# Kernel optimization log

Measured on AMD Instinct MI355X. Metric: run time of the kernel, lower is better.

Reference implementation:

```python
import jax, jax.numpy as jnp
import numpy as np

D_MODEL = 1024
NUM_HEADS = 16
D_HEAD = D_MODEL // NUM_HEADS
THETA = 10000.0
B, S = 2, 2048


def setup_inputs() -> dict:
    key = jax.random.key(0)
    ks = jax.random.split(key, 5)
    std = np.sqrt(2.0 / (D_MODEL + D_MODEL))
    x = jax.random.normal(ks[0], (B, S, D_MODEL), dtype=jnp.float32)
    Wq = jax.random.normal(ks[1], (D_MODEL, D_MODEL), dtype=jnp.float32) * std
    Wk = jax.random.normal(ks[2], (D_MODEL, D_MODEL), dtype=jnp.float32) * std
    Wv = jax.random.normal(ks[3], (D_MODEL, D_MODEL), dtype=jnp.float32) * std
    Wo = jax.random.normal(ks[4], (D_MODEL, D_MODEL), dtype=jnp.float32) * std
    token_positions = jnp.arange(S, dtype=jnp.int32)
    return {"x": x, "Wq": Wq, "Wk": Wk, "Wv": Wv, "Wo": Wo,
            "token_positions": token_positions}


def _apply_rope(t, token_positions):
    # t: [B, H, S, d_head]; interleaved (even/odd) RoPE
    dh = t.shape[-1]
    inv_freq = 1.0 / (THETA ** (jnp.arange(0, dh, 2, dtype=jnp.float32) / dh))
    freqs = token_positions.astype(jnp.float32)[:, None] * inv_freq  # [S, dh/2]
    cos = jnp.cos(freqs)  # broadcasts over B, H
    sin = jnp.sin(freqs)
    x1 = t[..., 0::2]
    x2 = t[..., 1::2]
    r1 = x1 * cos - x2 * sin
    r2 = x1 * sin + x2 * cos
    return jnp.stack([r1, r2], axis=-1).reshape(t.shape)


def reference(x, Wq, Wk, Wv, Wo, token_positions):
    b, s, d = x.shape
    h, dh = NUM_HEADS, D_HEAD

    def proj(W):
        y = x @ W.T  # [B, S, D]
        return y.reshape(b, s, h, dh).transpose(0, 2, 1, 3)  # [B, H, S, dh]

    q = _apply_rope(proj(Wq), token_positions)
    k = _apply_rope(proj(Wk), token_positions)
    v = proj(Wv)

    scores = jnp.einsum('bhqd,bhkd->bhqk', q, k) / jnp.sqrt(jnp.float32(dh))
    causal = jnp.tril(jnp.ones((s, s), dtype=bool))
    scores = jnp.where(causal, scores, jnp.float32(-jnp.inf))
    attn = jax.nn.softmax(scores, axis=-1)
    out = jnp.einsum('bhqk,bhkd->bhqd', attn, v)  # [B, H, S, dh]
    out = out.transpose(0, 2, 1, 3).reshape(b, s, d)
    return out @ Wo.T
```

## Files before the change

### kernel.cpp

```cpp
#include <hip/hip_runtime.h>
#include <hip/hip_bf16.h>
#include <math.h>

#define DMODEL 1024
#define NHEAD  16
#define DHEAD  64
#define BATCH  2
#define SEQ    2048
#define MROWS  (BATCH * SEQ)

typedef __attribute__((ext_vector_type(8))) __bf16 bf16x8;
typedef __attribute__((ext_vector_type(4))) float  f32x4;

__device__ __forceinline__ void load16_lds(const ushort* g, ushort* l) {
    __builtin_amdgcn_global_load_lds(
        (const __attribute__((address_space(1))) unsigned int*)g,
        (__attribute__((address_space(3))) unsigned int*)l, 16, 0, 0);
}

__device__ __forceinline__ ushort bf16u(float v) {
    __hip_bfloat16 h = __float2bfloat16(v);
    return *reinterpret_cast<ushort*>(&h);
}

__global__ __launch_bounds__(256)
void cast_f32_bf16(const float* __restrict__ s, ushort* __restrict__ d, int n) {
    const int i = (blockIdx.x * 256 + threadIdx.x) * 8;
    if (i >= n) return;
    const f32x4 a = *reinterpret_cast<const f32x4*>(s + i);
    const f32x4 b = *reinterpret_cast<const f32x4*>(s + i + 4);
    bf16x8 o;
    #pragma unroll
    for (int j = 0; j < 4; j++) { o[j] = (__bf16)a[j]; o[4 + j] = (__bf16)b[j]; }
    *reinterpret_cast<bf16x8*>(d + i) = o;
}

__global__ __launch_bounds__(256)
void cast_w4(const float* __restrict__ w0, const float* __restrict__ w1,
             const float* __restrict__ w2, const float* __restrict__ w3,
             ushort* __restrict__ dst) {
    const float* src = (blockIdx.y == 0) ? w0 : (blockIdx.y == 1) ? w1
                     : (blockIdx.y == 2) ? w2 : w3;
    const int i = (blockIdx.x * 256 + threadIdx.x) * 8;
    const f32x4 a = *reinterpret_cast<const f32x4*>(src + i);
    const f32x4 b = *reinterpret_cast<const f32x4*>(src + i + 4);
    bf16x8 o;
    #pragma unroll
    for (int j = 0; j < 4; j++) { o[j] = (__bf16)a[j]; o[4 + j] = (__bf16)b[j]; }
    *reinterpret_cast<bf16x8*>(dst + (size_t)blockIdx.y * DMODEL * DMODEL + i) = o;
}

__global__ __launch_bounds__(256)
void rope_tab(const int* __restrict__ pos, float2* __restrict__ tab) {
    const int idx = blockIdx.x * 256 + threadIdx.x;
    const int s = idx >> 5;
    const int i = idx & 31;
    const float p = (float)pos[s];
    const float inv = exp2f(-(float)i * 0.41524101186092f);
    float sn, cs;
    sincosf(p * inv, &sn, &cs);
    tab[idx] = make_float2(cs, sn);
}

#define QKV_BARRIER() do { asm volatile("" ::: "memory"); \
                           __builtin_amdgcn_s_barrier(); } while (0)

#define RD4(dst, p_)                                                          \
    _Pragma("unroll")                                                         \
    for (int rr_ = 0; rr_ < 4; rr_++)                                         \
        dst[rr_] = *reinterpret_cast<const bf16x8*>((p_) + rr_ * 512);

#define MFMA_G(AFR, BFR, IOFF)                                                \
    __builtin_amdgcn_s_setprio(1);                                            \
    _Pragma("unroll")                                                         \
    for (int im_ = 0; im_ < 4; im_++)                                         \
        _Pragma("unroll")                                                     \
        for (int jn_ = 0; jn_ < 4; jn_++)                                     \
            acc[(IOFF) + im_][jn_] = __builtin_amdgcn_mfma_f32_16x16x32_bf16( \
                AFR[im_], BFR[jn_], acc[(IOFF) + im_][jn_], 0, 0, 0);         \
    __builtin_amdgcn_s_setprio(0);

__global__ __launch_bounds__(512, 2)
void gemm_qkv(const ushort* __restrict__ A, const ushort* __restrict__ B,
              ushort* __restrict__ C, const float2* __restrict__ tab) {
    __shared__ __align__(16) ushort pool[65536];

    const int orig = blockIdx.y * gridDim.x + blockIdx.x;
    const int xcd  = orig & 7;
    const int ixd  = orig >> 3;
    const int by   = xcd * 2 + (ixd / 12);
    const int bx   = ixd % 12;
    const int m0   = by * 256;
    const int n0   = bx * 256;

    const int tid  = threadIdx.x;
    const int lane = tid & 63;
    const int w    = tid >> 6;
    const int l16  = lane & 15;
    const int quad = lane >> 4;
    const int wm   = (w >> 2) * 128;
    const int wn   = (w & 3) * 64;
    const int chq  = (quad ^ ((l16 & 3) ^ ((l16 & 4) >> 1))) << 3;
    const int srow = tid >> 2;
    const int ssc  = (tid & 3) ^ ((srow & 3) ^ ((srow & 4) >> 1));

    const ushort* gA = A + (size_t)(m0 + srow) * DMODEL + ssc * 8;
    const ushort* gB = B + (size_t)(n0 + srow) * DMODEL + ssc * 8;

    auto stageA = [&](int tt, int ks) {
        const int off = tt * 64 + ks * 32;
        const int lb  = ((tt & 1) << 15) + (ks << 13);
        load16_lds(gA + off,                &pool[lb + tid * 8]);
        load16_lds(gA + 128 * DMODEL + off, &pool[lb + 4096 + tid * 8]);
    };
    auto stageB = [&](int tt, int ks) {
        const int off = tt * 64 + ks * 32;
        const int lb  = ((tt & 1) << 15) + 16384 + (ks << 13);
        load16_lds(gB + off,                &pool[lb + tid * 8]);
        load16_lds(gB + 128 * DMODEL + off, &pool[lb + 4096 + tid * 8]);
    };

    stageA(0, 0); stageB(0, 0);
    stageA(0, 1); stageB(0, 1);
    stageA(1, 0); stageB(1, 0);

    f32x4 acc[8][4];
    #pragma unroll
    for (int i = 0; i < 8; i++)
        #pragma unroll
        for (int j = 0; j < 4; j++) acc[i][j] = (f32x4){0.f, 0.f, 0.f, 0.f};

    asm volatile("s_waitcnt vmcnt(4)" ::: "memory");
    __builtin_amdgcn_s_barrier();

    bf16x8 al[4], ah[4], bc[4], bn[4];

    { const ushort* p = pool + (wm + l16) * 32 + chq;           RD4(al, p); }
    { const ushort* q = pool + 16384 + (wn + l16) * 32 + chq;   RD4(bc, q); }

    #pragma unroll 1
    for (int t = 0; t < 16; t++) {
        const int buf  = (t & 1) << 15;
        const int bufn = buf ^ 32768;
        if (t <= 14) { stageA(t + 1, 1); stageB(t + 1, 1); }
        { const ushort* p = pool + buf + (wm + 64 + l16) * 32 + chq;
          RD4(ah, p); }
        MFMA_G(al, bc, 0);
        { const ushort* p = pool + buf + 8192 + (wm + l16) * 32 + chq;
          RD4(al, p);
          const ushort* q = pool + buf + 16384 + 8192 + (wn + l16) * 32 + chq;
          RD4(bn, q); }
        MFMA_G(ah, bc, 4);
        if (t <= 14) { asm volatile("s_waitcnt vmcnt(4)" ::: "memory"); }
        QKV_BARRIER();
        if (t <= 13) { stageA(t + 2, 0); stageB(t + 2, 0); }
        { const ushort* p = pool + buf + 8192 + (wm + 64 + l16) * 32 + chq;
          RD4(ah, p); }
        MFMA_G(al, bn, 0);
        if (t <= 14) {
            const ushort* p = pool + bufn + (wm + l16) * 32 + chq;
            RD4(al, p);
            const ushort* q = pool + bufn + 16384 + (wn + l16) * 32 + chq;
            RD4(bc, q);
        }
        MFMA_G(ah, bn, 4);
        if (t <= 13)      { asm volatile("s_waitcnt vmcnt(4)" ::: "memory"); }
        else if (t == 14) { asm volatile("s_waitcnt vmcnt(0)" ::: "memory"); }
        QKV_BARRIER();
    }

    const int nbase  = n0 + wn;
    const int tensor = nbase >> 10;
    const int hh     = (nbase & 1023) >> 6;
    if (tensor < 2) {
        ushort* Dt = C + (size_t)tensor * ((size_t)MROWS * DMODEL);
        #pragma unroll
        for (int i = 0; i < 8; i++)
            #pragma unroll
            for (int r = 0; r < 4; r++) {
                const int m  = m0 + wm + i * 16 + quad * 4 + r;
                const int bb = m >> 11;
                const int ss = m & (SEQ - 1);
                const float2* trow = tab + ss * 32;
                #pragma unroll
                for (int j = 0; j < 4; j++) {
                    const int f = j * 16 + l16;
                    const float2 cs = trow[f >> 1];
                    const float val = acc[i][j][r];
                    const float prt = __shfl_xor(val, 1, 64);
                    const float out = (f & 1) ? (prt * cs.y + val * cs.x)
                                              : (val * cs.x - prt * cs.y);
                    Dt[(((size_t)(bb * NHEAD + hh)) * SEQ + ss) * DHEAD + f] =
                        bf16u(out);
                }
            }
    } else {
        ushort* Tw = pool + w * 8192;
        #pragma unroll
        for (int i = 0; i < 8; i++)
            #pragma unroll
            for (int j = 0; j < 4; j++) {
                const int f  = j * 16 + l16;
                const int sx = (f & 7) << 3;
                #pragma unroll
                for (int r = 0; r < 4; r += 2) {
                    const int ml = i * 16 + quad * 4 + r;
                    ushort2 pk;
                    pk.x = bf16u(acc[i][j][r]);
                    pk.y = bf16u(acc[i][j][r + 1]);
                    *reinterpret_cast<ushort2*>(&Tw[f * 128 + (ml ^ sx)]) = pk;
                }
            }
        asm volatile("s_waitcnt lgkmcnt(0)" ::: "memory");
        ushort* Dv = C + 2 * ((size_t)MROWS * DMODEL);
        const int c  = lane & 15;
        const int fb = lane >> 4;
        #pragma unroll
        for (int rr = 0; rr < 16; rr++) {
            const int fl = rr * 4 + fb;
            const uint4 v = *reinterpret_cast<const uint4*>(
                &Tw[fl * 128 + ((c << 3) ^ ((fl & 7) << 3))]);
            *reinterpret_cast<uint4*>(
                &Dv[(size_t)(hh * 64 + fl) * MROWS + m0 + wm + (c << 3)]) = v;
        }
    }
}

__global__ __launch_bounds__(256)
void gemm_out64(const ushort* __restrict__ A, const ushort* __restrict__ B,
                float* __restrict__ C) {
    __shared__ __align__(16) ushort pool[12288];
    ushort* As = pool;
    ushort* Bs = pool + 4096;
    const int tid  = threadIdx.x;
    const int m0   = blockIdx.y * 64;
    const int n0   = blockIdx.x * 128;
    const int lane = tid & 63;
    const int w    = tid >> 6;
    const int l16  = lane & 15;
    const int quad = lane >> 4;
    const int wm   = (w >> 1) * 32;
    const int wn   = (w & 1) * 64;
    const int srow = tid >> 2;
    const int scol = (tid & 3) * 8;

    const int am  = m0 + srow;
    const int abb = am >> 11;
    const int ass = am & (SEQ - 1);
    const size_t abase = ((size_t)(abb * NHEAD)) * SEQ * DHEAD + (size_t)ass * DHEAD;

    f32x4 acc[2][4];
    #pragma unroll
    for (int i = 0; i < 2; i++)
        #pragma unroll
        for (int j = 0; j < 4; j++) acc[i][j] = (f32x4){0.f, 0.f, 0.f, 0.f};

    {
        const int h = scol >> 6, dh = scol & 63;
        load16_lds(A + abase + (size_t)h * SEQ * DHEAD + dh, &As[srow * 32 + scol]);
        #pragma unroll
        for (int half = 0; half < 2; half++) {
            const int row = srow + half * 64;
            load16_lds(B + (size_t)(n0 + row) * DMODEL + scol, &Bs[row * 32 + scol]);
        }
    }

    for (int t = 0; t < 32; t++) {
        const int bf = t & 1;
        __syncthreads();
        if (t + 1 < 32) {
            const int k0 = (t + 1) * 32;
            const int kk = k0 + scol;
            const int h = kk >> 6, dh = kk & 63;
            load16_lds(A + abase + (size_t)h * SEQ * DHEAD + dh,
                       &As[(bf ^ 1) * 2048 + srow * 32 + scol]);
            #pragma unroll
            for (int half = 0; half < 2; half++) {
                const int row = srow + half * 64;
                load16_lds(B + (size_t)(n0 + row) * DMODEL + k0 + scol,
                           &Bs[(bf ^ 1) * 4096 + row * 32 + scol]);
            }
        }
        const int oa = bf * 2048, ob_ = bf * 4096;
        bf16x8 af[2], bfr[4];
        #pragma unroll
        for (int s = 0; s < 2; s++)
            af[s] = *reinterpret_cast<const bf16x8*>(
                &As[oa + (wm + s * 16 + l16) * 32 + quad * 8]);
        #pragma unroll
        for (int s = 0; s < 4; s++)
            bfr[s] = *reinterpret_cast<const bf16x8*>(
                &Bs[ob_ + (wn + s * 16 + l16) * 32 + quad * 8]);
        #pragma unroll
        for (int i = 0; i < 2; i++)
            #pragma unroll
            for (int j = 0; j < 4; j++)
                acc[i][j] = __builtin_amdgcn_mfma_f32_16x16x32_bf16(
                    af[i], bfr[j], acc[i][j], 0, 0, 0);
    }
    #pragma unroll
    for (int i = 0; i < 2; i++)
        #pragma unroll
        for (int r = 0; r < 4; r++) {
            const int m = m0 + wm + i * 16 + quad * 4 + r;
            #pragma unroll
            for (int j = 0; j < 4; j++)
                C[(size_t)m * DMODEL + n0 + wn + j * 16 + l16] = acc[i][j][r];
        }
}

__global__ __launch_bounds__(256)
void attn_mfma6(const ushort* __restrict__ qb, const ushort* __restrict__ kb,
                const ushort* __restrict__ vtg, ushort* __restrict__ ob) {
    __shared__ __align__(16) ushort Ks[2][4096];
    __shared__ __align__(16) ushort Vs[2][4096];
    __shared__ ushort Pb[4][16][72];

    const int bh   = blockIdx.x;
    const int b    = bh >> 4;
    const int h    = bh & 15;
    const int qt   = (gridDim.y - 1) - blockIdx.y;
    const int tid  = threadIdx.x;
    const int w    = tid >> 6;
    const int lane = tid & 63;
    const int l16  = lane & 15;
    const int quad = lane >> 4;
    const size_t base = (size_t)bh * SEQ * DHEAD;

    const int qlo = qt * 64 + w * 16;

    const float SC = 0.125f * 1.44269504088896f;
    bf16x8 qa[2];
    {
        const size_t qo = base + (size_t)(qlo + l16) * DHEAD + quad * 8;
        qa[0] = *reinterpret_cast<const bf16x8*>(qb + qo);
        qa[1] = *reinterpret_cast<const bf16x8*>(qb + qo + 32);
        #pragma unroll
        for (int j = 0; j < 8; j++) {
            qa[0][j] = (__bf16)(SC * (float)qa[0][j]);
            qa[1][j] = (__bf16)(SC * (float)qa[1][j]);
        }
    }

    f32x4 oacc[4];
    #pragma unroll
    for (int s = 0; s < 4; s++) oacc[s] = (f32x4){0.f, 0.f, 0.f, 0.f};
    float l_ = 0.f;

    const int c0 = tid,        r0 = c0 >> 3, g0 = (c0 & 7) ^ (r0 & 7);
    const int c1 = 256 + tid,  r1 = c1 >> 3, g1 = (c1 & 7) ^ (r1 & 7);
    const ushort* kg0 = kb + base + (size_t)r0 * DHEAD + g0 * 8;
    const ushort* kg1 = kb + base + (size_t)r1 * DHEAD + g1 * 8;
    const ushort* vg0 = vtg + (size_t)(h * DHEAD + r0) * MROWS + b * SEQ + g0 * 8;
    const ushort* vg1 = vtg + (size_t)(h * DHEAD + r1) * MROWS + b * SEQ + g1 * 8;

    int koff[2][4];
    #pragma unroll
    for (int half = 0; half < 2; half++)
        #pragma unroll
        for (int sub = 0; sub < 4; sub++)
            koff[half][sub] = (sub * 16 + l16) * 64 +
                              (((half * 4 + quad) ^ (l16 & 7)) * 8);

    load16_lds(kg0, &Ks[0][c0 * 8]);
    load16_lds(kg1, &Ks[0][c1 * 8]);
    load16_lds(vg0, &Vs[0][c0 * 8]);
    load16_lds(vg1, &Vs[0][c1 * 8]);

    const int T = qt + 1;
    for (int t = 0; t < T; t++) {
        const int bf = t & 1;
        __syncthreads();
        if (t + 1 < T) {
            const size_t ko = (size_t)(t + 1) * 64 * DHEAD;
            const int    vo = (t + 1) * 64;
            load16_lds(kg0 + ko, &Ks[bf ^ 1][c0 * 8]);
            load16_lds(kg1 + ko, &Ks[bf ^ 1][c1 * 8]);
            load16_lds(vg0 + vo, &Vs[bf ^ 1][c0 * 8]);
            load16_lds(vg1 + vo, &Vs[bf ^ 1][c1 * 8]);
        }

        const bool diag = (t == qt);
        const int nsub = diag ? (w + 1) : 4;
        const int nhv  = diag ? ((w >> 1) + 1) : 2;

        f32x4 sacc[4];
        #pragma unroll
        for (int s = 0; s < 4; s++) sacc[s] = (f32x4){0.f, 0.f, 0.f, 0.f};
        #pragma unroll
        for (int half = 0; half < 2; half++)
            #pragma unroll
            for (int sub = 0; sub < 4; sub++)
                if (sub < nsub) {
                    const bf16x8 kf = *reinterpret_cast<const bf16x8*>(
                        &Ks[bf][koff[half][sub]]);
                    sacc[sub] = __builtin_amdgcn_mfma_f32_16x16x32_bf16(
                        kf, qa[half], sacc[sub], 0, 0, 0);
                }

        float ev[4][4];
        if (diag) {
            const int thr = qlo + l16 - t * 64;
            #pragma unroll
            for (int sub = 0; sub < 4; sub++)
                #pragma unroll
                for (int r = 0; r < 4; r++) {
                    const float e = (sub * 16 + quad * 4 + r <= thr)
                                        ? exp2f(sacc[sub][r]) : 0.f;
                    ev[sub][r] = e;
                    l_ += e;
                }
        } else {
            #pragma unroll
            for (int sub = 0; sub < 4; sub++)
                #pragma unroll
                for (int r = 0; r < 4; r++) {
                    const float e = exp2f(sacc[sub][r]);
                    ev[sub][r] = e;
                    l_ += e;
                }
        }

        #pragma unroll
        for (int sub = 0; sub < 4; sub++) {
            ushort4 pk;
            pk.x = bf16u(ev[sub][0]); pk.y = bf16u(ev[sub][1]);
            pk.z = bf16u(ev[sub][2]); pk.w = bf16u(ev[sub][3]);
            *reinterpret_cast<ushort4*>(&Pb[w][l16][sub * 16 + quad * 4]) = pk;
        }
        bf16x8 pa[2];
        pa[0] = *reinterpret_cast<const bf16x8*>(&Pb[w][l16][quad * 8]);
        pa[1] = *reinterpret_cast<const bf16x8*>(&Pb[w][l16][32 + quad * 8]);

        #pragma unroll
        for (int hk = 0; hk < 2; hk++) {
            if (hk >= nhv) break;
            #pragma unroll
            for (int sf = 0; sf < 4; sf++) {
                const bf16x8 vf = *reinterpret_cast<const bf16x8*>(
                    &Vs[bf][koff[hk][sf]]);
                oacc[sf] = __builtin_amdgcn_mfma_f32_16x16x32_bf16(
                    pa[hk], vf, oacc[sf], 0, 0, 0);
            }
        }
    }

    l_ += __shfl_xor(l_, 16, 64);
    l_ += __shfl_xor(l_, 32, 64);
    float inv[4];
    #pragma unroll
    for (int r = 0; r < 4; r++) inv[r] = 1.f / __shfl(l_, quad * 4 + r, 64);
    #pragma unroll
    for (int sub = 0; sub < 4; sub++)
        #pragma unroll
        for (int r = 0; r < 4; r++) {
            const int q = qlo + quad * 4 + r;
            ob[base + (size_t)q * DHEAD + sub * 16 + l16] =
                bf16u(oacc[sub][r] * inv[r]);
        }
}

extern "C" void kernel_launch(void* const* d_in, const int* in_sizes, int n_in,
                              void* d_out, int out_size, void* d_ws, size_t ws_size,
                              hipStream_t stream) {
    const float* x  = (const float*)d_in[0];
    const float* Wq = (const float*)d_in[1];
    const float* Wk = (const float*)d_in[2];
    const float* Wv = (const float*)d_in[3];
    const float* Wo = (const float*)d_in[4];
    const int* pos = (const int*)d_in[5];

    const size_t TEN = (size_t)MROWS * DMODEL;
    const size_t WEL = (size_t)DMODEL * DMODEL;
    ushort* xb   = (ushort*)d_ws;
    ushort* Wqkv = xb + TEN;
    ushort* Wob  = Wqkv + 3 * WEL;
    ushort* qb   = Wob + WEL;
    ushort* kb   = qb + TEN;
    ushort* vtb  = kb + TEN;
    ushort* ob   = vtb + TEN;
    float2* tab  = (float2*)(ob + TEN);

    dim3 blk(256);
    rope_tab<<<(SEQ * 32) / 256, blk, 0, stream>>>(pos, tab);
    cast_f32_bf16<<<TEN / (8 * 256), blk, 0, stream>>>(x, xb, (int)TEN);
    dim3 gcw(WEL / (8 * 256), 4);
    cast_w4<<<gcw, blk, 0, stream>>>(Wq, Wk, Wv, Wo, Wqkv);

    dim3 gqkv(3 * DMODEL / 256, MROWS / 256);
    gemm_qkv<<<gqkv, dim3(512), 0, stream>>>(xb, Wqkv, qb, tab);

    dim3 gattn(BATCH * NHEAD, SEQ / 64);
    attn_mfma6<<<gattn, blk, 0, stream>>>(qb, kb, vtb, ob);

    dim3 gout(DMODEL / 128, MROWS / 64);
    gemm_out64<<<gout, blk, 0, stream>>>(ob, Wob, (float*)d_out);
}
```

Measured before the change: 181.5 us.

## Transpose softmax probabilities via lane shuffles and compute row sums with MFMA

Removes the per-wave LDS staging buffer for the P matrix and instead repacks the exponentiated scores into the MFMA A-operand layout with cross-lane shuffles. The row-sum of probabilities is now accumulated by an extra MFMA against a vector of ones instead of scalar adds plus final cross-lane reductions. Launch bounds request 4 blocks per CU. This trades LDS writes and reads for eight shuffles per half, and one extra MFMA per half, and it sums the bf16-rounded probabilities rather than the fp32 ones.

Measured after the change: 188.7 us. +4.0%, slower.

```diff
diff --git a/kernel.cpp b/kernel.cpp
--- a/kernel.cpp
+++ b/kernel.cpp
@@ -21,6 +21,10 @@
 __device__ __forceinline__ ushort bf16u(float v) {
     __hip_bfloat16 h = __float2bfloat16(v);
     return *reinterpret_cast<ushort*>(&h);
+}
+
+__device__ __forceinline__ unsigned pack2bf(float a, float b) {
+    return (unsigned)bf16u(a) | ((unsigned)bf16u(b) << 16);
 }
 
 __global__ __launch_bounds__(256)
@@ -309,12 +313,11 @@
         }
 }
 
-__global__ __launch_bounds__(256)
-void attn_mfma6(const ushort* __restrict__ qb, const ushort* __restrict__ kb,
+__global__ __launch_bounds__(256, 4)
+void attn_mfma7(const ushort* __restrict__ qb, const ushort* __restrict__ kb,
                 const ushort* __restrict__ vtg, ushort* __restrict__ ob) {
     __shared__ __align__(16) ushort Ks[2][4096];
     __shared__ __align__(16) ushort Vs[2][4096];
-    __shared__ ushort Pb[4][16][72];
 
     const int bh   = blockIdx.x;
     const int b    = bh >> 4;
@@ -341,11 +344,14 @@
             qa[1][j] = (__bf16)(SC * (float)qa[1][j]);
         }
     }
+    bf16x8 onesb;
+    #pragma unroll
+    for (int j = 0; j < 8; j++) onesb[j] = (__bf16)1.0f;
 
     f32x4 oacc[4];
     #pragma unroll
     for (int s = 0; s < 4; s++) oacc[s] = (f32x4){0.f, 0.f, 0.f, 0.f};
-    float l_ = 0.f;
+    f32x4 lacc = (f32x4){0.f, 0.f, 0.f, 0.f};
 
     const int c0 = tid,        r0 = c0 >> 3, g0 = (c0 & 7) ^ (r0 & 7);
     const int c1 = 256 + tid,  r1 = c1 >> 3, g1 = (c1 & 7) ^ (r1 & 7);
@@ -361,6 +367,10 @@
         for (int sub = 0; sub < 4; sub++)
             koff[half][sub] = (sub * 16 + l16) * 64 +
                               (((half * 4 + quad) ^ (l16 & 7)) * 8);
+
+    const int srcA = l16 + ((quad & 1) << 5);
+    const int srcB = srcA + 16;
+    const bool hiSub = (quad & 2) != 0;
 
     load16_lds(kg0, &Ks[0][c0 * 8]);
     load16_lds(kg1, &Ks[0][c1 * 8]);
@@ -398,39 +408,49 @@
                         kf, qa[half], sacc[sub], 0, 0, 0);
                 }
 
-        float ev[4][4];
+        unsigned u0[4], u1[4];
         if (diag) {
             const int thr = qlo + l16 - t * 64;
             #pragma unroll
-            for (int sub = 0; sub < 4; sub++)
+            for (int sub = 0; sub < 4; sub++) {
+                float e[4];
                 #pragma unroll
-                for (int r = 0; r < 4; r++) {
-                    const float e = (sub * 16 + quad * 4 + r <= thr)
-                                        ? exp2f(sacc[sub][r]) : 0.f;
-                    ev[sub][r] = e;
-                    l_ += e;
-                }
+                for (int r = 0; r < 4; r++)
+                    e[r] = (sub * 16 + quad * 4 + r <= thr)
+                               ? exp2f(sacc[sub][r]) : 0.f;
+                u0[sub] = pack2bf(e[0], e[1]);
+                u1[sub] = pack2bf(e[2], e[3]);
+            }
         } else {
             #pragma unroll
-            for (int sub = 0; sub < 4; sub++)
+            for (int sub = 0; sub < 4; sub++) {
+                float e[4];
                 #pragma unroll
-                for (int r = 0; r < 4; r++) {
-                    const float e = exp2f(sacc[sub][r]);
-                    ev[sub][r] = e;
-                    l_ += e;
-                }
-        }
-
-        #pragma unroll
-        for (int sub = 0; sub < 4; sub++) {
-            ushort4 pk;
-            pk.x = bf16u(ev[sub][0]); pk.y = bf16u(ev[sub][1]);
-            pk.z = bf16u(ev[sub][2]); pk.w = bf16u(ev[sub][3]);
-            *reinterpret_cast<ushort4*>(&Pb[w][l16][sub * 16 + quad * 4]) = pk;
-        }
+                for (int r = 0; r < 4; r++) e[r] = exp2f(sacc[sub][r]);
+                u0[sub] = pack2bf(e[0], e[1]);
+                u1[sub] = pack2bf(e[2], e[3]);
+            }
+        }
+
         bf16x8 pa[2];
-        pa[0] = *reinterpret_cast<const bf16x8*>(&Pb[w][l16][quad * 8]);
-        pa[1] = *reinterpret_cast<const bf16x8*>(&Pb[w][l16][32 + quad * 8]);
+        #pragma unroll
+        for (int hk = 0; hk < 2; hk++) {
+            const int s0 = hk * 2, s1 = hk * 2 + 1;
+            const unsigned d0a = __shfl((int)u0[s0], srcA, 64);
+            const unsigned d0b = __shfl((int)u0[s1], srcA, 64);
+            const unsigned d1a = __shfl((int)u1[s0], srcA, 64);
+            const unsigned d1b = __shfl((int)u1[s1], srcA, 64);
+            const unsigned d2a = __shfl((int)u0[s0], srcB, 64);
+            const unsigned d2b = __shfl((int)u0[s1], srcB, 64);
+            const unsigned d3a = __shfl((int)u1[s0], srcB, 64);
+            const unsigned d3b = __shfl((int)u1[s1], srcB, 64);
+            uint4 dv;
+            dv.x = hiSub ? d0b : d0a;
+            dv.y = hiSub ? d1b : d1a;
+            dv.z = hiSub ? d2b : d2a;
+            dv.w = hiSub ? d3b : d3a;
+            pa[hk] = *reinterpret_cast<bf16x8*>(&dv);
+        }
 
         #pragma unroll
         for (int hk = 0; hk < 2; hk++) {
@@ -442,14 +462,14 @@
                 oacc[sf] = __builtin_amdgcn_mfma_f32_16x16x32_bf16(
                     pa[hk], vf, oacc[sf], 0, 0, 0);
             }
+            lacc = __builtin_amdgcn_mfma_f32_16x16x32_bf16(
+                pa[hk], onesb, lacc, 0, 0, 0);
         }
     }
 
-    l_ += __shfl_xor(l_, 16, 64);
-    l_ += __shfl_xor(l_, 32, 64);
     float inv[4];
     #pragma unroll
-    for (int r = 0; r < 4; r++) inv[r] = 1.f / __shfl(l_, quad * 4 + r, 64);
+    for (int r = 0; r < 4; r++) inv[r] = 1.f / lacc[r];
     #pragma unroll
     for (int sub = 0; sub < 4; sub++)
         #pragma unroll
@@ -491,7 +511,7 @@
     gemm_qkv<<<gqkv, dim3(512), 0, stream>>>(xb, Wqkv, qb, tab);
 
     dim3 gattn(BATCH * NHEAD, SEQ / 64);
-    attn_mfma6<<<gattn, blk, 0, stream>>>(qb, kb, vtb, ob);
+    attn_mfma7<<<gattn, blk, 0, stream>>>(qb, kb, vtb, ob);
 
     dim3 gout(DMODEL / 128, MROWS / 64);
     gemm_out64<<<gout, blk, 0, stream>>>(ob, Wob, (float*)d_out);
```

## Software-pipeline attention PV matmul one tile behind QK with triple-buffered V

Applied to the files above, without the earlier changes.

Restructures the attention loop so the P·V MFMA for tile t-1 is issued right after the QK^T MFMAs of tile t, before the exp/softmax of tile t. The MFMA work can then overlap with the transcendental and LDS round-trip for P, with a final epilogue PV step for the diagonal tile. V gets a third LDS buffer so the tile still being consumed is not overwritten by the prefetch. This raises LDS use and live registers (pa is carried across iterations), which could lower occupancy.

After: 191.7 us. 5.6% more time.

```diff
diff --git a/kernel.cpp b/kernel.cpp
--- a/kernel.cpp
+++ b/kernel.cpp
@@ -310,10 +310,10 @@
 }
 
 __global__ __launch_bounds__(256)
-void attn_mfma6(const ushort* __restrict__ qb, const ushort* __restrict__ kb,
+void attn_mfma8(const ushort* __restrict__ qb, const ushort* __restrict__ kb,
                 const ushort* __restrict__ vtg, ushort* __restrict__ ob) {
     __shared__ __align__(16) ushort Ks[2][4096];
-    __shared__ __align__(16) ushort Vs[2][4096];
+    __shared__ __align__(16) ushort Vs[3][4096];
     __shared__ ushort Pb[4][16][72];
 
     const int bh   = blockIdx.x;
@@ -346,6 +346,7 @@
     #pragma unroll
     for (int s = 0; s < 4; s++) oacc[s] = (f32x4){0.f, 0.f, 0.f, 0.f};
     float l_ = 0.f;
+    bf16x8 pa[2];
 
     const int c0 = tid,        r0 = c0 >> 3, g0 = (c0 & 7) ^ (r0 & 7);
     const int c1 = 256 + tid,  r1 = c1 >> 3, g1 = (c1 & 7) ^ (r1 & 7);
@@ -368,21 +369,22 @@
     load16_lds(vg1, &Vs[0][c1 * 8]);
 
     const int T = qt + 1;
+    #pragma unroll 1
     for (int t = 0; t < T; t++) {
-        const int bf = t & 1;
+        const int kbf = t & 1;
         __syncthreads();
         if (t + 1 < T) {
             const size_t ko = (size_t)(t + 1) * 64 * DHEAD;
             const int    vo = (t + 1) * 64;
-            load16_lds(kg0 + ko, &Ks[bf ^ 1][c0 * 8]);
-            load16_lds(kg1 + ko, &Ks[bf ^ 1][c1 * 8]);
-            load16_lds(vg0 + vo, &Vs[bf ^ 1][c0 * 8]);
-            load16_lds(vg1 + vo, &Vs[bf ^ 1][c1 * 8]);
+            const int    vs = (t + 1) % 3;
+            load16_lds(kg0 + ko, &Ks[kbf ^ 1][c0 * 8]);
+            load16_lds(kg1 + ko, &Ks[kbf ^ 1][c1 * 8]);
+            load16_lds(vg0 + vo, &Vs[vs][c0 * 8]);
+            load16_lds(vg1 + vo, &Vs[vs][c1 * 8]);
         }
 
         const bool diag = (t == qt);
         const int nsub = diag ? (w + 1) : 4;
-        const int nhv  = diag ? ((w >> 1) + 1) : 2;
 
         f32x4 sacc[4];
         #pragma unroll
@@ -393,10 +395,23 @@
             for (int sub = 0; sub < 4; sub++)
                 if (sub < nsub) {
                     const bf16x8 kf = *reinterpret_cast<const bf16x8*>(
-                        &Ks[bf][koff[half][sub]]);
+                        &Ks[kbf][koff[half][sub]]);
                     sacc[sub] = __builtin_amdgcn_mfma_f32_16x16x32_bf16(
                         kf, qa[half], sacc[sub], 0, 0, 0);
                 }
+
+        if (t > 0) {
+            const ushort* Vt = Vs[(t - 1) % 3];
+            #pragma unroll
+            for (int hk = 0; hk < 2; hk++)
+                #pragma unroll
+                for (int sf = 0; sf < 4; sf++) {
+                    const bf16x8 vf = *reinterpret_cast<const bf16x8*>(
+                        &Vt[koff[hk][sf]]);
+                    oacc[sf] = __builtin_amdgcn_mfma_f32_16x16x32_bf16(
+                        pa[hk], vf, oacc[sf], 0, 0, 0);
+                }
+        }
 
         float ev[4][4];
         if (diag) {
@@ -428,17 +443,20 @@
             pk.z = bf16u(ev[sub][2]); pk.w = bf16u(ev[sub][3]);
             *reinterpret_cast<ushort4*>(&Pb[w][l16][sub * 16 + quad * 4]) = pk;
         }
-        bf16x8 pa[2];
         pa[0] = *reinterpret_cast<const bf16x8*>(&Pb[w][l16][quad * 8]);
         pa[1] = *reinterpret_cast<const bf16x8*>(&Pb[w][l16][32 + quad * 8]);
-
+    }
+
+    {
+        const ushort* Vt = Vs[qt % 3];
+        const int nhv = (w >> 1) + 1;
         #pragma unroll
         for (int hk = 0; hk < 2; hk++) {
             if (hk >= nhv) break;
             #pragma unroll
             for (int sf = 0; sf < 4; sf++) {
                 const bf16x8 vf = *reinterpret_cast<const bf16x8*>(
-                    &Vs[bf][koff[hk][sf]]);
+                    &Vt[koff[hk][sf]]);
                 oacc[sf] = __builtin_amdgcn_mfma_f32_16x16x32_bf16(
                     pa[hk], vf, oacc[sf], 0, 0, 0);
             }
@@ -491,7 +509,7 @@
     gemm_qkv<<<gqkv, dim3(512), 0, stream>>>(xb, Wqkv, qb, tab);
 
     dim3 gattn(BATCH * NHEAD, SEQ / 64);
-    attn_mfma6<<<gattn, blk, 0, stream>>>(qb, kb, vtb, ob);
+    attn_mfma8<<<gattn, blk, 0, stream>>>(qb, kb, vtb, ob);
 
     dim3 gout(DMODEL / 128, MROWS / 64);
     gemm_out64<<<gout, blk, 0, stream>>>(ob, Wob, (float*)d_out);
```
